# Kernel optimization log

Measured on AMD Instinct MI355X. Metric: run time of the kernel, lower is better.

The kernel has to match this reference:

```python
import jax, jax.numpy as jnp
import numpy as np
import math

H = 12   # num_attention_heads
DH = 64  # attention_head_size
D = H * DH  # hidden_size = 768


def _split_heads(x):
    # [b, s, D] -> [b, H, s, DH]
    b, s, _ = x.shape
    return x.reshape(b, s, H, DH).transpose(0, 2, 1, 3)


def setup_inputs() -> dict:
    key = jax.random.key(0)
    ks = jax.random.split(key, 8)
    B, S, G, NUM_CTX = 32, 512, 16, 8
    real_b = B // NUM_CTX
    inp = {
        "hidden_states": jax.random.normal(ks[0], (B, S, D), dtype=jnp.float32),
        "attention_mask": jnp.zeros((B, 1, 1, S), dtype=jnp.float32),
        "global_tokens_embed": jax.random.normal(ks[1], (real_b, G, D), dtype=jnp.float32),
        "Wq": jax.random.normal(ks[2], (D, D), dtype=jnp.float32) * 0.02,
        "bq": jnp.zeros((D,), dtype=jnp.float32),
        "Wk": jax.random.normal(ks[3], (D, D), dtype=jnp.float32) * 0.02,
        "bk": jnp.zeros((D,), dtype=jnp.float32),
        "Wv": jax.random.normal(ks[4], (D, D), dtype=jnp.float32) * 0.02,
        "bv": jnp.zeros((D,), dtype=jnp.float32),
        "num_ctx": 8,
    }
    return inp


def reference(hidden_states, attention_mask, global_tokens_embed,
              Wq, bq, Wk, bk, Wv, bv, num_ctx):
    B, S, _ = hidden_states.shape
    real_b = B // num_ctx
    G = global_tokens_embed.shape[1]
    scale = 1.0 / math.sqrt(DH)

    # Q/K/V projections for packed contexts
    q = _split_heads(hidden_states @ Wq + bq)   # [B,H,S,DH]
    k = _split_heads(hidden_states @ Wk + bk)
    v = _split_heads(hidden_states @ Wv + bv)

    # Global token projections
    gq = _split_heads(global_tokens_embed @ Wq + bq)  # [real_b,H,G,DH]
    gk = _split_heads(global_tokens_embed @ Wk + bk)
    gv = _split_heads(global_tokens_embed @ Wv + bv)

    # ---- Global-token cross attention over all contexts of each real batch ----
    # [B,H,S,DH] -> [real_b, H, num_ctx*S, DH]
    full_k = k.transpose(0, 2, 1, 3).reshape(real_b, num_ctx * S, H, DH).transpose(0, 2, 1, 3)
    full_v = v.transpose(0, 2, 1, 3).reshape(real_b, num_ctx * S, H, DH).transpose(0, 2, 1, 3)
    full_k = jnp.concatenate([gk, full_k], axis=2)  # [real_b,H,G+num_ctx*S,DH]
    full_v = jnp.concatenate([gv, full_v], axis=2)

    g_scores = jnp.einsum('bhgd,bhkd->bhgk', gq, full_k) * scale
    g_mask = attention_mask.reshape(real_b, num_ctx * S)[:, None, None, :]
    g_mask = jnp.concatenate([jnp.zeros((real_b, 1, 1, G), g_mask.dtype), g_mask], axis=3)
    g_scores = g_scores + g_mask
    g_probs = jax.nn.softmax(g_scores, axis=-1)
    g_ctx = jnp.einsum('bhgk,bhkd->bhgd', g_probs, full_v)
    g_ctx = g_ctx.transpose(0, 2, 1, 3).reshape(real_b, G, D)  # [real_b,G,D]

    # ---- Local attention: each context attends to its own tokens + global tokens ----
    gk_rep = jnp.broadcast_to(gk[:, None], (real_b, num_ctx, H, G, DH)).reshape(B, H, G, DH)
    gv_rep = jnp.broadcast_to(gv[:, None], (real_b, num_ctx, H, G, DH)).reshape(B, H, G, DH)
    k2 = jnp.concatenate([gk_rep, k], axis=2)  # [B,H,G+S,DH]
    v2 = jnp.concatenate([gv_rep, v], axis=2)
    mask2 = jnp.concatenate([jnp.zeros((B, 1, 1, G), attention_mask.dtype), attention_mask], axis=3)

    scores = jnp.einsum('bhqd,bhkd->bhqk', q, k2) * scale + mask2  # [B,H,S,G+S]
    probs = jax.nn.softmax(scores, axis=-1)
    ctx = jnp.einsum('bhqk,bhkd->bhqd', probs, v2)
    ctx = ctx.transpose(0, 2, 1, 3).reshape(B, S, D)  # [B,S,D]

    return ctx, g_ctx
```

## Files before the change

### kernel.cpp

```cpp
#include <hip/hip_runtime.h>
#include <hip/hip_bf16.h>
#include <stdint.h>

#define NH 12
#define DHD 64
#define DM 768
#define BB 32
#define SS 512
#define GG 16
#define NCTX 8
#define RBATCH 4
#define OUTG_OFF ((size_t)BB * SS * DM)

#define XROWS 16512
#define NALL 2304
#define NX8 (XROWS * DM / 8)
#define NB8 (NALL / 8)
#define NM8 (BB * SS / 8)

#define LOG2E 1.4426950408889634f
#define QSCALE 0.18033688011112042f

typedef __bf16 bf16x8 __attribute__((ext_vector_type(8)));
typedef float f32x4 __attribute__((ext_vector_type(4)));
typedef float f32x16 __attribute__((ext_vector_type(16)));

__device__ __forceinline__ float b2f(unsigned short u) {
    union { unsigned int i; float f; } x;
    x.i = ((unsigned int)u) << 16;
    return x.f;
}
__device__ __forceinline__ unsigned short f2b(float f) {
    __hip_bfloat16 h = __float2bfloat16(f);
    return *reinterpret_cast<unsigned short*>(&h);
}
__device__ __forceinline__ unsigned int pk2(float a, float b) {
    return ((unsigned int)f2b(b) << 16) | (unsigned int)f2b(a);
}
__device__ __forceinline__ float ex2(float x) {
    return __builtin_amdgcn_exp2f(x);
}
__device__ __forceinline__ float ldv(const void* p, size_t i, int isf32) {
    return isf32 ? ((const float*)p)[i] : b2f(((const unsigned short*)p)[i]);
}
__device__ __forceinline__ void stv(void* p, size_t i, int isf32, float v) {
    if (isf32) ((float*)p)[i] = v;
    else       ((unsigned short*)p)[i] = f2b(v);
}
__device__ __forceinline__ void async_cp16(const unsigned short* g, unsigned short* l) {
    __builtin_amdgcn_global_load_lds(
        (const __attribute__((address_space(1))) unsigned int*)g,
        (__attribute__((address_space(3))) unsigned int*)l, 16, 0, 0);
}

__device__ __forceinline__ void vt_pair_store(unsigned int* Vt32, int vr, int scc,
                                              uint4 a, uint4 b, int ldq) {
    const unsigned int* au = (const unsigned int*)&a;
    const unsigned int* bu = (const unsigned int*)&b;
    #pragma unroll
    for (int i = 0; i < 4; i++) {
        const int d0 = scc + 2 * i;
        const int swz = ((vr >> 3) ^ ((d0 >> 3) & 7));
        const int i32 = d0 * ldq + (swz << 2) + ((vr & 7) >> 1);
        Vt32[i32]       = __builtin_amdgcn_perm(bu[i], au[i], 0x05040100u);
        Vt32[i32 + ldq] = __builtin_amdgcn_perm(bu[i], au[i], 0x07060302u);
    }
}

__global__ __launch_bounds__(256) void detect_dtype(
    const unsigned short* __restrict__ Wq, int* __restrict__ flag)
{
    __shared__ int hi, zz;
    if (threadIdx.x == 0) { hi = 0; zz = 0; }
    __syncthreads();
    int lh = 0, lz = 0;
    for (int i = threadIdx.x; i < 4096; i += 256) {
        unsigned short u = Wq[2 * i];
        if (((u >> 7) & 0xFF) >= 130) lh++;
        if (u == 0) lz++;
    }
    atomicAdd(&hi, lh);
    atomicAdd(&zz, lz);
    __syncthreads();
    if (threadIdx.x == 0) *flag = (hi > 512 || zz > 3500) ? 1 : 0;
}

__global__ __launch_bounds__(256) void cvt_x(
    const void* __restrict__ hs, const void* __restrict__ gte,
    const void* __restrict__ bq, const void* __restrict__ bk,
    const void* __restrict__ bv, const void* __restrict__ mask,
    const int* __restrict__ flag,
    unsigned short* __restrict__ Xb, unsigned short* __restrict__ b_all,
    unsigned short* __restrict__ wmask)
{
    const int e = blockIdx.x * 256 + threadIdx.x;
    const int isf32 = *flag;
    if (e < NX8) {
        const int base = e * 8;
        const int row = base / DM, col = base % DM;
        unsigned short o8[8];
        if (row < 16384) {
            if (isf32) {
                float4 a = ((const float4*)hs)[e * 2];
                float4 c = ((const float4*)hs)[e * 2 + 1];
                o8[0]=f2b(a.x); o8[1]=f2b(a.y); o8[2]=f2b(a.z); o8[3]=f2b(a.w);
                o8[4]=f2b(c.x); o8[5]=f2b(c.y); o8[6]=f2b(c.z); o8[7]=f2b(c.w);
            } else {
                *(uint4*)o8 = ((const uint4*)hs)[e];
            }
        } else if (row < 16448) {
            size_t soff = (size_t)(row - 16384) * DM + col;
            #pragma unroll
            for (int i = 0; i < 8; i++) o8[i] = f2b(ldv(gte, soff + i, isf32));
        } else {
            #pragma unroll
            for (int i = 0; i < 8; i++) o8[i] = 0;
        }
        *(uint4*)&Xb[base] = *(const uint4*)o8;
    } else if (e < NX8 + NB8) {
        const int i0 = (e - NX8) * 8;
        #pragma unroll
        for (int i = 0; i < 8; i++) {
            int ng = i0 + i;
            int z = ng / DM;
            const void* src = (z == 0) ? bq : (z == 1) ? bk : bv;
            b_all[ng] = f2b(ldv(src, ng % DM, isf32));
        }
    } else if (e < NX8 + NB8 + NM8) {
        const int i0 = (e - NX8 - NB8) * 8;
        #pragma unroll
        for (int i = 0; i < 8; i++)
            wmask[i0 + i] = f2b(ldv(mask, i0 + i, isf32) * LOG2E);
    }
}

__global__ __launch_bounds__(256) void cvt_w(
    const void* __restrict__ Wq, const void* __restrict__ Wk,
    const void* __restrict__ Wv, const int* __restrict__ flag,
    unsigned short* __restrict__ Wt)
{
    __shared__ float T[64][65];
    const int kt = blockIdx.x;
    const int ngt = blockIdx.y;
    const int z = ngt / 12, nt = ngt % 12;
    const int tid = threadIdx.x;
    const int isf32 = *flag;
    const void* W = (z == 0) ? Wq : (z == 1) ? Wk : Wv;

    for (int jj = 0; jj < 16; jj++) {
        int el = tid + jj * 256;
        int r = el >> 6, c = el & 63;
        T[r][c] = ldv(W, (size_t)(kt * 64 + r) * DM + nt * 64 + c, isf32);
    }
    __syncthreads();
    for (int jj = 0; jj < 16; jj++) {
        int el = tid + jj * 256;
        int rn = el >> 6, ck = el & 63;
        Wt[(size_t)(z * DM + nt * 64 + rn) * DM + kt * 64 + ck] = f2b(T[ck][rn]);
    }
}

#define QKV_NWG (129 * 18)
__global__ __launch_bounds__(256) void qkv_gemm(
    const unsigned short* __restrict__ Xb,
    const unsigned short* __restrict__ Wt,
    const unsigned short* __restrict__ b_all,
    unsigned short* __restrict__ q, unsigned short* __restrict__ kk_,
    unsigned short* __restrict__ v,
    unsigned short* __restrict__ gq, unsigned short* __restrict__ gk,
    unsigned short* __restrict__ gv)
{
    __shared__ __align__(16) unsigned short As[2][2][128 * 32];
    __shared__ __align__(16) unsigned short Bs[2][2][128 * 32];

    const int orig = blockIdx.x;
    const int q8 = QKV_NWG >> 3, r8 = QKV_NWG & 7;
    const int xcd = orig & 7, lin = orig >> 3;
    const int swz = (xcd < r8 ? xcd * (q8 + 1) : r8 * (q8 + 1) + (xcd - r8) * q8) + lin;
    const int mt = swz / 18, nt = swz - mt * 18;

    const int tid = threadIdx.x;
    const int wave = tid >> 6, lane = tid & 63;
    const int quad = lane >> 4, l16 = lane & 15;
    const int wm = wave & 1, wn = wave >> 1;
    const int z = nt / 6;
    unsigned short* YL = (z == 0) ? q : (z == 1) ? kk_ : v;
    unsigned short* YG = (z == 0) ? gq : (z == 1) ? gk : gv;
    const float qsc = (z == 0) ? QSCALE : 1.0f;

    const int sr = tid >> 2, sc = (tid & 3) * 8;

    const unsigned short* Arow0 = &Xb[(size_t)(mt * 128 + sr) * DM + sc];
    const unsigned short* Arow1 = Arow0 + (size_t)64 * DM;
    const unsigned short* Brow0 = &Wt[(size_t)(nt * 128 + sr) * DM + sc];
    const unsigned short* Brow1 = Brow0 + (size_t)64 * DM;

    f32x4 acc[4][4];
    #pragma unroll
    for (int i = 0; i < 4; i++)
        for (int j = 0; j < 4; j++)
            for (int r = 0; r < 4; r++) acc[i][j][r] = 0.f;

#define QKV_STAGE_PAIR(p, bb) do {                                       \
        const int k0_ = (p) * 64;                                        \
        async_cp16(Arow0 + k0_,      &As[(bb)][0][wave * 512]);          \
        async_cp16(Arow1 + k0_,      &As[(bb)][0][2048 + wave * 512]);   \
        async_cp16(Brow0 + k0_,      &Bs[(bb)][0][wave * 512]);          \
        async_cp16(Brow1 + k0_,      &Bs[(bb)][0][2048 + wave * 512]);   \
        async_cp16(Arow0 + k0_ + 32, &As[(bb)][1][wave * 512]);          \
        async_cp16(Arow1 + k0_ + 32, &As[(bb)][1][2048 + wave * 512]);   \
        async_cp16(Brow0 + k0_ + 32, &Bs[(bb)][1][wave * 512]);          \
        async_cp16(Brow1 + k0_ + 32, &Bs[(bb)][1][2048 + wave * 512]);   \
    } while (0)

    QKV_STAGE_PAIR(0, 0);
    __syncthreads();

    int cur = 0;
    for (int p = 0; p < 12; p++) {
        if (p < 11) QKV_STAGE_PAIR(p + 1, cur ^ 1);

        #pragma unroll
        for (int sub = 0; sub < 2; sub++) {
            bf16x8 af[4], bf[4];
            #pragma unroll
            for (int ib = 0; ib < 4; ib++)
                af[ib] = *(const bf16x8*)&As[cur][sub][(wm * 64 + ib * 16 + l16) * 32 + quad * 8];
            #pragma unroll
            for (int jb = 0; jb < 4; jb++)
                bf[jb] = *(const bf16x8*)&Bs[cur][sub][(wn * 64 + jb * 16 + l16) * 32 + quad * 8];
            #pragma unroll
            for (int ib = 0; ib < 4; ib++)
                #pragma unroll
                for (int jb = 0; jb < 4; jb++)
                    acc[ib][jb] = __builtin_amdgcn_mfma_f32_16x16x32_bf16(
                        bf[jb], af[ib], acc[ib][jb], 0, 0, 0);
        }

        if (p < 11) __syncthreads();
        cur ^= 1;
    }
#undef QKV_STAGE_PAIR

    #pragma unroll
    for (int ib = 0; ib < 4; ib++) {
        const int m = mt * 128 + wm * 64 + ib * 16 + l16;
        if (m >= 16448) continue;
        const bool loc = (m < 16384);
        const int b = m >> 9, s = m & 511;
        const int gl = m - 16384;
        const int rbx = gl >> 4, g = gl & 15;
        #pragma unroll
        for (int jb = 0; jb < 4; jb++) {
            const int ng0 = nt * 128 + wn * 64 + jb * 16 + quad * 4;
            const int o = ng0 - z * DM;
            const int h = o >> 6, dh0 = o & 63;
            const uint2 bu = *(const uint2*)&b_all[ng0];
            const unsigned short* bp = (const unsigned short*)&bu;
            const float y0 = (acc[ib][jb][0] + b2f(bp[0])) * qsc;
            const float y1 = (acc[ib][jb][1] + b2f(bp[1])) * qsc;
            const float y2 = (acc[ib][jb][2] + b2f(bp[2])) * qsc;
            const float y3 = (acc[ib][jb][3] + b2f(bp[3])) * qsc;
            uint2 o2;
            o2.x = pk2(y0, y1);
            o2.y = pk2(y2, y3);
            if (loc) {
                *(uint2*)&YL[(((size_t)b * NH + h) * SS + s) * DHD + dh0] = o2;
            } else {
                *(uint2*)&YG[(((size_t)rbx * NH + h) * GG + g) * DHD + dh0] = o2;
            }
        }
    }
}

#define AL_NWG (4 * NH * BB)
__global__ __launch_bounds__(256) void attn_local(
    const unsigned short* __restrict__ q,
    const unsigned short* __restrict__ k,
    const unsigned short* __restrict__ v,
    const unsigned short* __restrict__ gk,
    const unsigned short* __restrict__ gv,
    const unsigned short* __restrict__ wmask,
    const int* __restrict__ flag,
    void* __restrict__ out)
{
    __shared__ __align__(16) unsigned short Ks[64 * 64];
    __shared__ __align__(16) unsigned short Vt[64 * 64];

    const int orig = blockIdx.x;
    const int swz = (orig & 7) * (AL_NWG / 8) + (orig >> 3);
    const int qt = swz & 3;
    const int hb = swz >> 2;
    const int h = hb % NH, b = hb / NH;

    const int rb = b >> 3;
    const int tid = threadIdx.x, wave = tid >> 6, lane = tid & 63;
    const int l31 = lane & 31, h8 = lane >> 5;
    const int isf32 = *flag;
    const int q0 = qt * 128 + wave * 32;

    const size_t bh = (size_t)b * NH + h;
    const unsigned short* qp = q + bh * SS * DHD;
    const unsigned short* kp = k + bh * SS * DHD;
    const unsigned short* vp = v + bh * SS * DHD;
    const size_t gbh = (size_t)rb * NH + h;
    const unsigned short* gkp = gk + gbh * GG * DHD;
    const unsigned short* gvp = gv + gbh * GG * DHD;

    bf16x8 qf[4];
    #pragma unroll
    for (int kb = 0; kb < 4; kb++)
        qf[kb] = *(const bf16x8*)&qp[(size_t)(q0 + l31) * DHD + kb * 16 + h8 * 8];

    f32x16 oacc[2];
    #pragma unroll
    for (int mb = 0; mb < 2; mb++)
        #pragma unroll
        for (int j = 0; j < 16; j++) oacc[mb][j] = 0.f;
    float m_s = -1e30f, l_s = 0.f;

    const int sr = tid >> 3, scc = (tid & 7) * 8;
    const int vr = sr * 2;
    const int agc = (((lane & 7) ^ ((lane >> 3) & 7)) << 3);
    const int arow = 8 * wave + (lane >> 3);
    unsigned int* Vt32 = (unsigned int*)Vt;

    for (int t = 0; t < 9; t++) {
        __syncthreads();
        if (t == 0) {
            if (sr < 16) {
                uint4 kx = *(const uint4*)&gkp[sr * DHD + scc];
                *(uint4*)&Ks[sr * 64 + (((scc >> 3) ^ (sr & 7)) << 3)] = kx;
            } else {
                uint4 zz4 = {0, 0, 0, 0};
                *(uint4*)&Ks[sr * 64 + (((scc >> 3) ^ (sr & 7)) << 3)] = zz4;
            }
            uint4 va = {0, 0, 0, 0}, vb = {0, 0, 0, 0};
            if (sr < 8) {
                va = *(const uint4*)&gvp[vr * DHD + scc];
                vb = *(const uint4*)&gvp[(vr + 1) * DHD + scc];
            }
            vt_pair_store(Vt32, vr, scc, va, vb, 32);
        } else {
            const int ks0 = (t - 1) * 64;
            #pragma unroll
            for (int p = 0; p < 2; p++)
                async_cp16(&kp[(size_t)(ks0 + p * 32 + arow) * DHD + agc],
                           &Ks[p * 2048 + wave * 512]);
            uint4 va = *(const uint4*)&vp[(size_t)(ks0 + vr) * DHD + scc];
            uint4 vb = *(const uint4*)&vp[(size_t)(ks0 + vr + 1) * DHD + scc];
            vt_pair_store(Vt32, vr, scc, va, vb, 32);
        }
        __syncthreads();

        f32x16 scA, scB;
        #pragma unroll
        for (int kt = 0; kt < 2; kt++) {
            f32x16 cc;
            #pragma unroll
            for (int j = 0; j < 16; j++) cc[j] = 0.f;
            if (kt == 0 || t > 0) {
                #pragma unroll
                for (int kb = 0; kb < 4; kb++) {
                    const int key = kt * 32 + l31;
                    bf16x8 kf = *(const bf16x8*)&Ks[key * 64 + (((kb * 2 + h8) ^ (key & 7)) << 3)];
                    cc = __builtin_amdgcn_mfma_f32_32x32x16_bf16(kf, qf[kb], cc, 0, 0, 0);
                }
                if (t > 0) {
                    #pragma unroll
                    for (int rg = 0; rg < 4; rg++) {
                        uint2 mu = *(const uint2*)&wmask[b * SS + (t - 1) * 64 + kt * 32 + rg * 8 + 4 * h8];
                        const unsigned short* mp = (const unsigned short*)&mu;
                        #pragma unroll
                        for (int r = 0; r < 4; r++)
                            cc[rg * 4 + r] += b2f(mp[r]);
                    }
                } else {
                    #pragma unroll
                    for (int j = 8; j < 16; j++) cc[j] = -1e30f;
                }
            } else {
                #pragma unroll
                for (int j = 0; j < 16; j++) cc[j] = -1e30f;
            }
            if (kt == 0) scA = cc; else scB = cc;
        }

        float mx = -1e30f;
        #pragma unroll
        for (int j = 0; j < 16; j++) mx = fmaxf(mx, scA[j]);
        #pragma unroll
        for (int j = 0; j < 16; j++) mx = fmaxf(mx, scB[j]);
        mx = fmaxf(mx, __shfl_xor(mx, 32, 64));
        if (!__all(mx <= m_s)) {
            const float mn = fmaxf(m_s, mx);
            const float alpha = ex2(m_s - mn);
            m_s = mn;
            l_s *= alpha;
            #pragma unroll
            for (int mb = 0; mb < 2; mb++)
                #pragma unroll
                for (int j = 0; j < 16; j++) oacc[mb][j] *= alpha;
        }
        float rs = 0.f;
        #pragma unroll
        for (int j = 0; j < 16; j++) { float pw = ex2(scA[j] - m_s); scA[j] = pw; rs += pw; }
        #pragma unroll
        for (int j = 0; j < 16; j++) { float pw = ex2(scB[j] - m_s); scB[j] = pw; rs += pw; }
        rs += __shfl_xor(rs, 32, 64);
        l_s += rs;

        #pragma unroll
        for (int kt = 0; kt < 2; kt++) {
            unsigned int wA[4], wB[4];
            #pragma unroll
            for (int g = 0; g < 4; g++) {
                const float s0 = (kt == 0) ? scA[4 * g + 0] : scB[4 * g + 0];
                const float s1 = (kt == 0) ? scA[4 * g + 1] : scB[4 * g + 1];
                const float s2 = (kt == 0) ? scA[4 * g + 2] : scB[4 * g + 2];
                const float s3 = (kt == 0) ? scA[4 * g + 3] : scB[4 * g + 3];
                wA[g] = pk2(s0, s1);
                wB[g] = pk2(s2, s3);
            }
            #pragma unroll
            for (int kb = 0; kb < 2; kb++) {
                auto ra  = __builtin_amdgcn_permlane32_swap(wA[2 * kb], wA[2 * kb + 1], false, false);
                auto rbp = __builtin_amdgcn_permlane32_swap(wB[2 * kb], wB[2 * kb + 1], false, false);
                union { unsigned int u[4]; bf16x8 v8; } pfu;
                pfu.u[0] = (unsigned int)ra[0];
                pfu.u[1] = (unsigned int)rbp[0];
                pfu.u[2] = (unsigned int)ra[1];
                pfu.u[3] = (unsigned int)rbp[1];
                const int kb2 = kt * 2 + kb;
                #pragma unroll
                for (int mb = 0; mb < 2; mb++) {
                    const int d = mb * 32 + l31;
                    bf16x8 vf = *(const bf16x8*)&Vt[d * 64 + (((kb2 * 2 + h8) ^ ((d >> 3) & 7)) << 3)];
                    oacc[mb] = __builtin_amdgcn_mfma_f32_32x32x16_bf16(vf, pfu.v8, oacc[mb], 0, 0, 0);
                }
            }
        }
    }

    const float inv = 1.f / l_s;
    const int s = q0 + l31;
    #pragma unroll
    for (int mb = 0; mb < 2; mb++) {
        #pragma unroll
        for (int rg = 0; rg < 4; rg++) {
            const int d0 = mb * 32 + rg * 8 + 4 * h8;
            const size_t idx = ((size_t)b * SS + s) * DM + h * DHD + d0;
            if (isf32) {
                float4 o4;
                o4.x = oacc[mb][rg * 4 + 0] * inv;
                o4.y = oacc[mb][rg * 4 + 1] * inv;
                o4.z = oacc[mb][rg * 4 + 2] * inv;
                o4.w = oacc[mb][rg * 4 + 3] * inv;
                *(float4*)&((float*)out)[idx] = o4;
            } else {
                uint2 o2;
                o2.x = pk2(oacc[mb][rg * 4 + 0] * inv, oacc[mb][rg * 4 + 1] * inv);
                o2.y = pk2(oacc[mb][rg * 4 + 2] * inv, oacc[mb][rg * 4 + 3] * inv);
                *(uint2*)&((unsigned short*)out)[idx] = o2;
            }
        }
    }
}

__global__ __launch_bounds__(256) void attn_gsplit(
    const unsigned short* __restrict__ k,
    const unsigned short* __restrict__ v,
    const unsigned short* __restrict__ gq,
    const unsigned short* __restrict__ gk,
    const unsigned short* __restrict__ gv,
    const unsigned short* __restrict__ wmask,
    float* __restrict__ Opart, float* __restrict__ Mpart,
    float* __restrict__ Lpart)
{
    __shared__ __align__(16) unsigned short Ks[128 * 64];
    __shared__ __align__(16) unsigned short Vt[64 * 128];
    __shared__ __align__(16) unsigned short Ps[4 * 16 * 64];

    const int h = blockIdx.x, rb = blockIdx.y, sp = blockIdx.z;
    const int tid = threadIdx.x, wave = tid >> 6, lane = tid & 63;
    const int quad = lane >> 4, l16 = lane & 15;

    const size_t gbh = (size_t)rb * NH + h;
    const unsigned short* gqp = gq + gbh * GG * DHD;
    const unsigned short* gkp = gk + gbh * GG * DHD;
    const unsigned short* gvp = gv + gbh * GG * DHD;

    bf16x8 aq[2];
    aq[0] = *(const bf16x8*)&gqp[l16 * DHD + quad * 8];
    aq[1] = *(const bf16x8*)&gqp[l16 * DHD + 32 + quad * 8];

    f32x4 oacc[4];
    #pragma unroll
    for (int db = 0; db < 4; db++)
        for (int r = 0; r < 4; r++) oacc[db][r] = 0.f;
    float m_s = -1e30f, l_s = 0.f;

    const int sr = tid >> 3, scc = (tid & 7) * 8;
    const int vr = sr * 2;
    const int agc = (((lane & 7) ^ ((lane >> 3) & 7)) << 3);
    const int arow = 8 * wave + (lane >> 3);
    unsigned short* myP = &Ps[wave * 1024];
    unsigned int* Vt32 = (unsigned int*)Vt;

    const int nt = (sp == 0) ? 9 : 8;
    for (int ti = 0; ti < nt; ti++) {
        const bool gtile = (sp == 0 && ti == 0);
        int cb = 0, soff = 0;
        __syncthreads();
        if (gtile) {
            if (sr < 16) {
                uint4 kx = *(const uint4*)&gkp[sr * DHD + scc];
                *(uint4*)&Ks[sr * 64 + (((scc >> 3) ^ (sr & 7)) << 3)] = kx;
                uint4 va = {0, 0, 0, 0}, vb = {0, 0, 0, 0};
                if (sr < 8) {
                    va = *(const uint4*)&gvp[vr * DHD + scc];
                    vb = *(const uint4*)&gvp[(vr + 1) * DHD + scc];
                }
                vt_pair_store(Vt32, vr, scc, va, vb, 64);
            } else {
                uint4 zz4 = {0, 0, 0, 0};
                *(uint4*)&Ks[sr * 64 + (((scc >> 3) ^ (sr & 7)) << 3)] = zz4;
            }
        } else {
            const int kidx = sp * 1024 + (ti - ((sp == 0) ? 1 : 0)) * 128;
            cb = rb * NCTX + (kidx >> 9);
            soff = kidx & 511;
            const unsigned short* kp = k + ((size_t)cb * NH + h) * SS * DHD;
            const unsigned short* vp = v + ((size_t)cb * NH + h) * SS * DHD;
            #pragma unroll
            for (int p = 0; p < 4; p++)
                async_cp16(&kp[(size_t)(soff + p * 32 + arow) * DHD + agc],
                           &Ks[p * 2048 + wave * 512]);
            #pragma unroll
            for (int pp = 0; pp < 2; pp++) {
                const int vrr = vr + pp * 64;
                uint4 va = *(const uint4*)&vp[(size_t)(soff + vrr) * DHD + scc];
                uint4 vb = *(const uint4*)&vp[(size_t)(soff + vrr + 1) * DHD + scc];
                vt_pair_store(Vt32, vrr, scc, va, vb, 64);
            }
        }
        __syncthreads();

        if (gtile && wave != 0) continue;

        const int nbn = gtile ? 1 : 2;
        f32x4 c[2];
        for (int hh = 0; hh < nbn; hh++) {
            f32x4 cc = {0.f, 0.f, 0.f, 0.f};
            const int key = wave * 32 + hh * 16 + l16;
            #pragma unroll
            for (int kd = 0; kd < 2; kd++) {
                bf16x8 kf = *(const bf16x8*)&Ks[key * 64 + (((kd * 4 + quad) ^ (key & 7)) << 3)];
                cc = __builtin_amdgcn_mfma_f32_16x16x32_bf16(kf, aq[kd], cc, 0, 0, 0);
            }
            if (!gtile) {
                uint2 mu = *(const uint2*)&wmask[cb * SS + soff + wave * 32 + hh * 16 + quad * 4];
                const unsigned short* mp = (const unsigned short*)&mu;
                #pragma unroll
                for (int r = 0; r < 4; r++)
                    cc[r] += b2f(mp[r]);
            }
            c[hh] = cc;
        }

        float mx = -1e30f;
        for (int hh = 0; hh < nbn; hh++)
            #pragma unroll
            for (int r = 0; r < 4; r++) mx = fmaxf(mx, c[hh][r]);
        mx = fmaxf(mx, __shfl_xor(mx, 16, 64));
        mx = fmaxf(mx, __shfl_xor(mx, 32, 64));
        const float mn = fmaxf(m_s, mx);
        const float alpha = ex2(m_s - mn);
        m_s = mn;
        float rs = 0.f;
        for (int hh = 0; hh < nbn; hh++)
            #pragma unroll
            for (int r = 0; r < 4; r++) {
                float p = ex2(c[hh][r] - mn);
                c[hh][r] = p;
                rs += p;
            }
        rs += __shfl_xor(rs, 16, 64);
        rs += __shfl_xor(rs, 32, 64);
        l_s = l_s * alpha + rs;
        #pragma unroll
        for (int db = 0; db < 4; db++)
            for (int r = 0; r < 4; r++) oacc[db][r] *= alpha;

        for (int hh = 0; hh < nbn; hh++) {
            uint2 pw;
            pw.x = pk2(c[hh][0], c[hh][1]);
            pw.y = pk2(c[hh][2], c[hh][3]);
            const int cch = ((hh * 2 + (quad >> 1)) ^ (l16 & 7));
            *(uint2*)&myP[l16 * 64 + cch * 8 + (quad & 1) * 4] = pw;
        }
        if (nbn == 1) {
            uint2 zz2; zz2.x = 0; zz2.y = 0;
            const int cch = ((2 + (quad >> 1)) ^ (l16 & 7));
            *(uint2*)&myP[l16 * 64 + cch * 8 + (quad & 1) * 4] = zz2;
        }

        bf16x8 pf = *(const bf16x8*)&myP[l16 * 64 + ((quad ^ (l16 & 7)) << 3)];
        #pragma unroll
        for (int db = 0; db < 4; db++) {
            const int d = db * 16 + l16;
            const int kc = wave * 4 + quad;
            bf16x8 vf = *(const bf16x8*)&Vt[d * 128 + ((kc ^ ((d >> 3) & 7)) << 3)];
            oacc[db] = __builtin_amdgcn_mfma_f32_16x16x32_bf16(vf, pf, oacc[db], 0, 0, 0);
        }
    }

    __syncthreads();
    float* Om = (float*)Ks;
    float* Mw = (float*)Vt;
    float* Lw = Mw + 64;
    #pragma unroll
    for (int db = 0; db < 4; db++)
        for (int r = 0; r < 4; r++)
            Om[(wave * 16 + l16) * 64 + db * 16 + quad * 4 + r] = oacc[db][r];
    if (quad == 0) {
        Mw[wave * 16 + l16] = m_s;
        Lw[wave * 16 + l16] = l_s;
    }
    __syncthreads();

    const size_t pbase = ((size_t)(sp * RBATCH + rb) * NH + h) * 1024;
    for (int e = tid; e < 1024; e += 256) {
        const int qrow = e >> 6, d = e & 63;
        float M = fmaxf(fmaxf(Mw[qrow], Mw[16 + qrow]), fmaxf(Mw[32 + qrow], Mw[48 + qrow]));
        float acc = 0.f, L = 0.f;
        #pragma unroll
        for (int w = 0; w < 4; w++) {
            float scw = ex2(Mw[w * 16 + qrow] - M);
            acc += Om[(w * 16 + qrow) * 64 + d] * scw;
            L += Lw[w * 16 + qrow] * scw;
        }
        Opart[pbase + e] = acc;
        if (d == 0) {
            Mpart[((sp * RBATCH + rb) * NH + h) * 16 + qrow] = M;
            Lpart[((sp * RBATCH + rb) * NH + h) * 16 + qrow] = L;
        }
    }
}

__global__ __launch_bounds__(256) void attn_gmerge(
    const float* __restrict__ Opart, const float* __restrict__ Mpart,
    const float* __restrict__ Lpart, const int* __restrict__ flag,
    void* __restrict__ out)
{
    const int h = blockIdx.x, rb = blockIdx.y;
    const int tid = threadIdx.x;
    const int isf32 = *flag;
    for (int e = tid; e < 1024; e += 256) {
        const int qrow = e >> 6, d = e & 63;
        float M = -1e30f;
        #pragma unroll
        for (int sp = 0; sp < 4; sp++)
            M = fmaxf(M, Mpart[((sp * RBATCH + rb) * NH + h) * 16 + qrow]);
        float acc = 0.f, L = 0.f;
        #pragma unroll
        for (int sp = 0; sp < 4; sp++) {
            const size_t pb = ((size_t)(sp * RBATCH + rb) * NH + h);
            float scs = ex2(Mpart[pb * 16 + qrow] - M);
            acc += Opart[pb * 1024 + e] * scs;
            L += Lpart[pb * 16 + qrow] * scs;
        }
        stv(out, OUTG_OFF + ((size_t)rb * GG + qrow) * DM + h * DHD + d, isf32, acc / L);
    }
}

extern "C" void kernel_launch(void* const* d_in, const int* in_sizes, int n_in,
                              void* d_out, int out_size, void* d_ws, size_t ws_size,
                              hipStream_t stream) {
    const void* hs   = d_in[0];
    const void* mask = d_in[1];
    const void* gte  = d_in[2];
    const void* Wq   = d_in[3];
    const void* bq   = d_in[4];
    const void* Wk   = d_in[5];
    const void* bk   = d_in[6];
    const void* Wv   = d_in[7];
    const void* bv   = d_in[8];

    const size_t qkv_sz = (size_t)BB * NH * SS * DHD;
    const size_t g_sz   = (size_t)RBATCH * NH * GG * DHD;
    const size_t msk_sz = (size_t)BB * SS;
    const size_t x_sz   = (size_t)XROWS * DM;
    const size_t wt_sz  = (size_t)NALL * DM;
    const size_t ba_sz  = (size_t)NALL;
    const size_t need_hw = 3 * qkv_sz + 3 * g_sz + msk_sz + x_sz + wt_sz + ba_sz;
    if (ws_size < need_hw * 2 + 16) return;

    unsigned short* q     = (unsigned short*)d_ws;
    unsigned short* kk    = q + qkv_sz;
    unsigned short* vv    = kk + qkv_sz;
    unsigned short* gq    = vv + qkv_sz;
    unsigned short* gk    = gq + g_sz;
    unsigned short* gv    = gk + g_sz;
    unsigned short* wmask = gv + g_sz;
    unsigned short* Xb    = wmask + msk_sz;
    unsigned short* Wt    = Xb + x_sz;
    unsigned short* b_all = Wt + wt_sz;
    int* flag = (int*)(b_all + ba_sz);
    float* Opart = (float*)Xb;
    float* Mpart = Opart + 4 * RBATCH * NH * 1024;
    float* Lpart = Mpart + 4 * RBATCH * NH * 16;

    detect_dtype<<<1, 256, 0, stream>>>((const unsigned short*)Wq, flag);

    const int cvt_items = NX8 + NB8 + NM8;
    cvt_x<<<(cvt_items + 255) / 256, 256, 0, stream>>>(
        hs, gte, bq, bk, bv, mask, flag, Xb, b_all, wmask);
    cvt_w<<<dim3(12, 36), 256, 0, stream>>>(Wq, Wk, Wv, flag, Wt);

    qkv_gemm<<<dim3(QKV_NWG), 256, 0, stream>>>(Xb, Wt, b_all, q, kk, vv, gq, gk, gv);

    attn_local<<<dim3(AL_NWG), 256, 0, stream>>>(
        q, kk, vv, gk, gv, wmask, flag, d_out);
    attn_gsplit<<<dim3(NH, RBATCH, 4), 256, 0, stream>>>(
        kk, vv, gq, gk, gv, wmask, Opart, Mpart, Lpart);
    attn_gmerge<<<dim3(NH, RBATCH), 256, 0, stream>>>(
        Opart, Mpart, Lpart, flag, d_out);
}
```

Measured before the change: 332.6 us.

## Double-buffer K/V shared tiles in local attention to overlap loads with compute

The local attention kernel now keeps two K and two transposed-V tiles in LDS. The global-token tile is staged before the loop, and each iteration issues the async K copy and the V global loads for the next tile before the MFMA work on the current one. The V transpose store and a single barrier follow the compute. This removes one of the two barriers per iteration and hides global-load latency behind compute, at the cost of doubling LDS use (which may lower occupancy) and holding V registers live across the compute.

Result: no change. 332.9 us (+0.1%).

```diff
diff --git a/kernel.cpp b/kernel.cpp
--- a/kernel.cpp
+++ b/kernel.cpp
@@ -284,8 +284,8 @@
     const int* __restrict__ flag,
     void* __restrict__ out)
 {
-    __shared__ __align__(16) unsigned short Ks[64 * 64];
-    __shared__ __align__(16) unsigned short Vt[64 * 64];
+    __shared__ __align__(16) unsigned short Ks[2][64 * 64];
+    __shared__ __align__(16) unsigned short Vt[2][64 * 64];
 
     const int orig = blockIdx.x;
     const int swz = (orig & 7) * (AL_NWG / 8) + (orig >> 3);
@@ -323,35 +323,39 @@
     const int vr = sr * 2;
     const int agc = (((lane & 7) ^ ((lane >> 3) & 7)) << 3);
     const int arow = 8 * wave + (lane >> 3);
-    unsigned int* Vt32 = (unsigned int*)Vt;
+
+    if (sr < 16) {
+        uint4 kx = *(const uint4*)&gkp[sr * DHD + scc];
+        *(uint4*)&Ks[0][sr * 64 + (((scc >> 3) ^ (sr & 7)) << 3)] = kx;
+    } else {
+        uint4 zz4 = {0, 0, 0, 0};
+        *(uint4*)&Ks[0][sr * 64 + (((scc >> 3) ^ (sr & 7)) << 3)] = zz4;
+    }
+    {
+        uint4 va0 = {0, 0, 0, 0}, vb0 = {0, 0, 0, 0};
+        if (sr < 8) {
+            va0 = *(const uint4*)&gvp[vr * DHD + scc];
+            vb0 = *(const uint4*)&gvp[(vr + 1) * DHD + scc];
+        }
+        vt_pair_store((unsigned int*)Vt[0], vr, scc, va0, vb0, 32);
+    }
+    __syncthreads();
 
     for (int t = 0; t < 9; t++) {
-        __syncthreads();
-        if (t == 0) {
-            if (sr < 16) {
-                uint4 kx = *(const uint4*)&gkp[sr * DHD + scc];
-                *(uint4*)&Ks[sr * 64 + (((scc >> 3) ^ (sr & 7)) << 3)] = kx;
-            } else {
-                uint4 zz4 = {0, 0, 0, 0};
-                *(uint4*)&Ks[sr * 64 + (((scc >> 3) ^ (sr & 7)) << 3)] = zz4;
-            }
-            uint4 va = {0, 0, 0, 0}, vb = {0, 0, 0, 0};
-            if (sr < 8) {
-                va = *(const uint4*)&gvp[vr * DHD + scc];
-                vb = *(const uint4*)&gvp[(vr + 1) * DHD + scc];
-            }
-            vt_pair_store(Vt32, vr, scc, va, vb, 32);
-        } else {
-            const int ks0 = (t - 1) * 64;
+        const int cur = t & 1;
+        const unsigned short* KsC = Ks[cur];
+        const unsigned short* VtC = Vt[cur];
+
+        uint4 va, vb;
+        if (t < 8) {
+            const int ks0 = t * 64;
+            va = *(const uint4*)&vp[(size_t)(ks0 + vr) * DHD + scc];
+            vb = *(const uint4*)&vp[(size_t)(ks0 + vr + 1) * DHD + scc];
             #pragma unroll
             for (int p = 0; p < 2; p++)
                 async_cp16(&kp[(size_t)(ks0 + p * 32 + arow) * DHD + agc],
-                           &Ks[p * 2048 + wave * 512]);
-            uint4 va = *(const uint4*)&vp[(size_t)(ks0 + vr) * DHD + scc];
-            uint4 vb = *(const uint4*)&vp[(size_t)(ks0 + vr + 1) * DHD + scc];
-            vt_pair_store(Vt32, vr, scc, va, vb, 32);
-        }
-        __syncthreads();
+                           &Ks[cur ^ 1][p * 2048 + wave * 512]);
+        }
 
         f32x16 scA, scB;
         #pragma unroll
@@ -363,7 +367,7 @@
                 #pragma unroll
                 for (int kb = 0; kb < 4; kb++) {
                     const int key = kt * 32 + l31;
-                    bf16x8 kf = *(const bf16x8*)&Ks[key * 64 + (((kb * 2 + h8) ^ (key & 7)) << 3)];
+                    bf16x8 kf = *(const bf16x8*)&KsC[key * 64 + (((kb * 2 + h8) ^ (key & 7)) << 3)];
                     cc = __builtin_amdgcn_mfma_f32_32x32x16_bf16(kf, qf[kb], cc, 0, 0, 0);
                 }
                 if (t > 0) {
@@ -435,10 +439,15 @@
                 #pragma unroll
                 for (int mb = 0; mb < 2; mb++) {
                     const int d = mb * 32 + l31;
-                    bf16x8 vf = *(const bf16x8*)&Vt[d * 64 + (((kb2 * 2 + h8) ^ ((d >> 3) & 7)) << 3)];
+                    bf16x8 vf = *(const bf16x8*)&VtC[d * 64 + (((kb2 * 2 + h8) ^ ((d >> 3) & 7)) << 3)];
                     oacc[mb] = __builtin_amdgcn_mfma_f32_32x32x16_bf16(vf, pfu.v8, oacc[mb], 0, 0, 0);
                 }
             }
+        }
+
+        if (t < 8) {
+            vt_pair_store((unsigned int*)Vt[cur ^ 1], vr, scc, va, vb, 32);
+            __syncthreads();
         }
     }
 
```
